# Performance work log

Hardware: AMD Instinct MI355X
Metric: run time of the kernel (lower is better)

Reference implementation:

```python
import jax, jax.numpy as jnp
import numpy as np

MASK_RADIUS = 30.0

def _lowpass_mask(H, W):
    cht, cwt = H // 2, W // 2
    fy = jnp.arange(H, dtype=jnp.float32)[:, None]
    fx = jnp.arange(W, dtype=jnp.float32)[None, :]
    dist = jnp.sqrt((fx - cwt) ** 2 + (fy - cht) ** 2)
    return (dist <= MASK_RADIUS).astype(jnp.float32)

def setup_inputs() -> dict:
    key = jax.random.key(0)
    k1, k2, k3 = jax.random.split(key, 3)
    x = jax.random.normal(k1, (16, 64, 128, 128), dtype=jnp.float32)
    weight = jax.random.normal(k2, (64, 64, 3, 3), dtype=jnp.float32)
    bias = jax.random.normal(k3, (64,), dtype=jnp.float32)
    return {"x": x, "weight": weight, "bias": bias}

def reference(x, weight, bias):
    B, Cin, H, W = x.shape
    # torch.fft.fftshift default shifts ALL dims; jnp default matches.
    fft_x = jnp.fft.fftshift(jnp.fft.fft2(x))                    # [B,Cin,H,W] complex
    kernel_fft = jnp.fft.fftshift(jnp.fft.fft2(weight, s=(H, W)))  # [Cout,Cin,H,W] complex
    # low-pass filter in the shifted frequency domain
    fft_x = fft_x * _lowpass_mask(H, W)
    # channel mixing = batched complex GEMM per frequency (avoids [B,Cout,Cin,H,W] intermediate)
    fft_out = jnp.einsum('bihw,oihw->bohw', fft_x, kernel_fft)
    out = jnp.fft.ifft2(jnp.fft.ifftshift(fft_out, axes=(-2, -1)), axes=(-2, -1)).real
    return out + bias[None, :, None, None]
```

## Files before the change

kernel.cpp:

```cpp
#include <hip/hip_runtime.h>


#define PI2_128 0.04908738521234052f
#define NF 1891

typedef __attribute__((ext_vector_type(8))) short bf16x8;
typedef __attribute__((ext_vector_type(4))) float f32x4;

__device__ const int k_flist[64] = {
    2, 6, 10, 14, 18, 22, 26, 30, 34, 38, 42, 46, 50, 54, 58,
    3, 7, 11, 15, 19, 23, 27, 31, 35, 39, 43, 47, 51, 55, 59,
    0, 4, 8, 12, 16, 20, 24, 28, 32, 36, 40, 44, 48, 52, 56, 60,
    1, 5, 9, 13, 17, 21, 25, 29, 33, 37, 41, 45, 49, 53, 57,
    0, 0, 0};

__device__ inline unsigned bf16_rne(float v) {
  unsigned u = __float_as_uint(v);
  return (u + 0x7FFFu + ((u >> 16) & 1u)) >> 16;
}

__device__ inline bf16x8 mk_bf16x8(unsigned a, unsigned b, unsigned c, unsigned d) {
  union { unsigned u[4]; bf16x8 v; } x;
  x.u[0] = a; x.u[1] = b; x.u[2] = c; x.u[3] = d;
  return x.v;
}

__global__ __launch_bounds__(256) void k0_what(const float* __restrict__ w,
                                               unsigned* __restrict__ Wt) {
  const int tid = threadIdx.x;
  const int fxp = blockIdx.x >> 4;
  const int ig = blockIdx.x & 15;
  const int il = tid & 3;
  const int o = ((tid >> 5) << 3) | ((tid >> 2) & 7);
  const int i = ig * 4 + il;
  const int op = (o + 32) & 63;
  const float* wp = w + (size_t)(op * 64 + i) * 9;
  float w9[9];
#pragma unroll
  for (int k = 0; k < 9; ++k) w9[k] = wp[k];

  const float fx = (float)(fxp - 30);
  float sn, cs;
  __sincosf(fx * PI2_128, &sn, &cs);
  const float e1x = cs, e1y = -sn;
  const float e2x = e1x * e1x - e1y * e1y, e2y = 2.f * e1x * e1y;
  float rxr[3], rxi[3];
#pragma unroll
  for (int ky = 0; ky < 3; ++ky) {
    rxr[ky] = w9[ky * 3] + w9[ky * 3 + 1] * e1x + w9[ky * 3 + 2] * e2x;
    rxi[ky] = w9[ky * 3 + 1] * e1y + w9[ky * 3 + 2] * e2y;
  }
  float pyx = 1.f, pyy = 0.f;
  const float stx = 0.9987954562f, sty = -0.04906767433f;
  unsigned* Wb = Wt + (size_t)(fxp * 31) * 4096 + (o >> 3) * 512 + (i >> 4) * 128 +
                 (((i >> 2) & 3) * 8 + (o & 7)) * 4 + (i & 3);
  for (int fy = 0; fy < 31; ++fy) {
    float p2x = pyx * pyx - pyy * pyy, p2y = 2.f * pyx * pyy;
    float Wre = rxr[0] + (rxr[1] * pyx - rxi[1] * pyy) + (rxr[2] * p2x - rxi[2] * p2y);
    float Wim = rxi[0] + (rxr[1] * pyy + rxi[1] * pyx) + (rxr[2] * p2y + rxi[2] * p2x);
    Wb[(size_t)fy * 4096] = bf16_rne(Wre) | (bf16_rne(Wim) << 16);
    float nx = pyx * stx - pyy * sty;
    pyy = pyx * sty + pyy * stx;
    pyx = nx;
  }
}

__global__ __launch_bounds__(256) void k12_fwd(const float* __restrict__ x,
                                               float* __restrict__ X2) {
  __shared__ __align__(16) float Cls[8968];
  const int bi = blockIdx.x;
  const int tid = threadIdx.x;
  const float* img = x + (size_t)bi * 16384;

  {
    const int tg = tid >> 5;
    const int xg = tid & 31;
    const int t_[4] = {4 * tg, 4 * tg + 2, 2 * tg + 1, 2 * tg + 17};
    const float sgn = (tg & 1) ? 1.f : -1.f;
    float pc[4], ps[4], stc[4], sts[4];
#pragma unroll
    for (int f = 0; f < 4; ++f) {
      __sincosf((float)t_[f] * PI2_128, &sts[f], &stc[f]);
      pc[f] = 1.f;
      ps[f] = 0.f;
    }
    float ar_[4][4] = {{0.f}}, ai_[4][4] = {{0.f}};
    for (int y = 0; y < 32; ++y) {
      float v[4][4];
#pragma unroll
      for (int k = 0; k < 4; ++k)
#pragma unroll
        for (int m = 0; m < 4; ++m) v[k][m] = img[(y + 32 * k) * 128 + xg + 32 * m];
#pragma unroll
      for (int m = 0; m < 4; ++m) {
        float s = v[0][m] + v[2][m], d = v[0][m] - v[2][m];
        float s2 = v[1][m] + v[3][m], d2 = (v[1][m] - v[3][m]) * sgn;
        float a0 = s + s2, a1 = s - s2;
        ar_[0][m] += a0 * pc[0];
        ai_[0][m] -= a0 * ps[0];
        ar_[1][m] += a1 * pc[1];
        ai_[1][m] -= a1 * ps[1];
        ar_[2][m] += d * pc[2] + d2 * ps[2];
        ai_[2][m] += -d * ps[2] + d2 * pc[2];
        ar_[3][m] += d * pc[3] + d2 * ps[3];
        ai_[3][m] += -d * ps[3] + d2 * pc[3];
      }
#pragma unroll
      for (int f = 0; f < 4; ++f) {
        float c = pc[f], s = ps[f];
        pc[f] = c * stc[f] - s * sts[f];
        ps[f] = s * stc[f] + c * sts[f];
      }
    }
#pragma unroll
    for (int f = 0; f < 4; ++f) {
      int t = t_[f];
      float Ar = ar_[f][0] + ar_[f][2], Ai = ai_[f][0] + ai_[f][2];
      float Br = ar_[f][0] - ar_[f][2], Bi = ai_[f][0] - ai_[f][2];
      float Cr = ar_[f][1] + ar_[f][3], Ci = ai_[f][1] + ai_[f][3];
      float Dr = ar_[f][1] - ar_[f][3], Di = ai_[f][1] - ai_[f][3];
      float* base = Cls + xg * 70 + 2 * t;
      *(float2*)(base + 0 * 2244) = make_float2(Ar + Cr, Ai + Ci);
      *(float2*)(base + 1 * 2244) = make_float2(Br + Di, Bi - Dr);
      *(float2*)(base + 2 * 2244) = make_float2(Ar - Cr, Ai - Ci);
      *(float2*)(base + 3 * 2244) = make_float2(Br - Di, Bi + Dr);
    }
  }
  __syncthreads();

  {
    const int tg2 = tid >> 5;
    const int fxg = tid & 31;
    float accr[2][4] = {{0.f}}, acci[2][4] = {{0.f}};
    int fxp_[2], r_[2];
    float pc2[2], ps2[2], stc2[2], sts2[2];
#pragma unroll
    for (int u = 0; u < 2; ++u) {
      fxp_[u] = k_flist[2 * fxg + u];
      r_[u] = (fxp_[u] + 2) & 3;
      float fx = (float)(fxp_[u] - 30);
      __sincosf(fx * PI2_128, &sts2[u], &stc2[u]);
      pc2[u] = 1.f;
      ps2[u] = 0.f;
    }
    for (int xx = 0; xx < 32; ++xx) {
#pragma unroll
      for (int u = 0; u < 2; ++u) {
        const float* bp = Cls + r_[u] * 2244 + xx * 70 + 8 * tg2;
        float2 p0 = *(const float2*)(bp);
        float2 p1 = *(const float2*)(bp + 2);
        float2 p2 = *(const float2*)(bp + 4);
        float2 p3 = *(const float2*)(bp + 6);
        float zr[4] = {p0.x, p1.x, p2.x, p3.x};
        float zi[4] = {p0.y, p1.y, p2.y, p3.y};
        float c = pc2[u], s = ps2[u];
#pragma unroll
        for (int tt = 0; tt < 4; ++tt) {
          accr[u][tt] += zr[tt] * c + zi[tt] * s;
          acci[u][tt] += zi[tt] * c - zr[tt] * s;
        }
        pc2[u] = c * stc2[u] - s * sts2[u];
        ps2[u] = s * stc2[u] + c * sts2[u];
      }
    }
    float2* X2c = (float2*)X2 + (size_t)bi * NF;
#pragma unroll
    for (int u = 0; u < 2; ++u) {
      if (2 * fxg + u >= 61) continue;
      int fxp = fxp_[u], fx = fxp - 30;
#pragma unroll
      for (int tt = 0; tt < 4; ++tt) {
        int t = 4 * tg2 + tt;
        if (t >= 31) continue;
        bool keep = (t * t + fx * fx) <= 900;
        X2c[fxp * 31 + t] =
            keep ? make_float2(accr[u][tt], acci[u][tt]) : make_float2(0.f, 0.f);
      }
    }
  }
}

__global__ __launch_bounds__(256) void ktx(const float2* __restrict__ X2,
                                           float2* __restrict__ X2T) {
  __shared__ __align__(16) float2 Ld[4096];
  const int tid = threadIdx.x;
  const int tf = blockIdx.x % 30;
  const int tc = blockIdx.x / 30;
  const int f2_0 = tf * 64;
  const int lo = tid & 63, hi = tid >> 6;
#pragma unroll
  for (int k = 0; k < 16; ++k) {
    int c = k * 4 + hi;
    int bi = (c & 15) * 64 + tc * 4 + (c >> 4);
    int f2 = f2_0 + lo;
    float2 v = (f2 < NF) ? X2[(size_t)bi * NF + f2] : make_float2(0.f, 0.f);
    Ld[(c << 6) | (lo ^ c)] = v;
  }
  __syncthreads();
#pragma unroll
  for (int k = 0; k < 16; ++k) {
    int fr = k * 4 + hi;
    int f2 = f2_0 + fr;
    if (f2 < NF) X2T[(size_t)f2 * 1024 + tc * 64 + lo] = Ld[(lo << 6) | (fr ^ lo)];
  }
}

__global__ __launch_bounds__(256) void k3_mfma(const float* X2T,
                                               const unsigned* __restrict__ WtB,
                                               float* F) {
  const int nwg = (int)gridDim.x;
  const int orig = (int)blockIdx.x;
  const int xcd = orig & 7;
  const int q = nwg >> 3, r = nwg & 7;
  const int blk = (xcd < r ? xcd * (q + 1) : r * (q + 1) + (xcd - r) * q) + (orig >> 3);

  const int tid = (int)threadIdx.x;
  const int wv = tid >> 6;
  const int g = blk * 4 + wv;
  const int f2v = g >> 1;
  const bool valid = f2v < NF;
  const int f2 = valid ? f2v : NF - 1;
  const int half = g & 1;
  const int lane = tid & 63;
  const int m = lane & 15;
  const int lg = lane >> 4;
  const int bs = (m + 8) & 15;
  const int co = m & 1;

  float2 xv[4][4];
  const float2* Xc = (const float2*)X2T;
#pragma unroll
  for (int ks = 0; ks < 4; ++ks)
#pragma unroll
    for (int t = 0; t < 4; ++t)
      xv[ks][t] = Xc[(size_t)f2 * 1024 + (ks * 16 + lg * 4 + t) * 16 + bs];

  __syncthreads();

  unsigned ahi[4][4], alo[4][4];
#pragma unroll
  for (int ks = 0; ks < 4; ++ks) {
#pragma unroll
    for (int t = 0; t < 4; ++t) {
      float xr = xv[ks][t].x, xi = xv[ks][t].y;
      unsigned hr = bf16_rne(xr), hi2 = bf16_rne(xi);
      float lr = xr - __uint_as_float(hr << 16);
      float li = xi - __uint_as_float(hi2 << 16);
      ahi[ks][t] = hr | (hi2 << 16);
      alo[ks][t] = bf16_rne(lr) | (bf16_rne(li) << 16);
    }
  }

  f32x4 acc[4];
#pragma unroll
  for (int nt = 0; nt < 4; ++nt) acc[nt] = {0.f, 0.f, 0.f, 0.f};

  const unsigned* Wb =
      WtB + (size_t)f2 * 4096 + half * 2048 + (lg * 8 + (m >> 1)) * 4;
#pragma unroll
  for (int ks = 0; ks < 4; ++ks) {
    bf16x8 bfr[4];
#pragma unroll
    for (int nt = 0; nt < 4; ++nt) {
      uint4 wq = *(const uint4*)(Wb + nt * 512 + ks * 128);
      unsigned b0, b1, b2, b3;
      if (co) {
        b0 = (wq.x >> 16) | (wq.x << 16);
        b1 = (wq.y >> 16) | (wq.y << 16);
        b2 = (wq.z >> 16) | (wq.z << 16);
        b3 = (wq.w >> 16) | (wq.w << 16);
      } else {
        b0 = wq.x ^ 0x80000000u;
        b1 = wq.y ^ 0x80000000u;
        b2 = wq.z ^ 0x80000000u;
        b3 = wq.w ^ 0x80000000u;
      }
      bfr[nt] = mk_bf16x8(b0, b1, b2, b3);
    }
    bf16x8 ah = mk_bf16x8(ahi[ks][0], ahi[ks][1], ahi[ks][2], ahi[ks][3]);
    bf16x8 al = mk_bf16x8(alo[ks][0], alo[ks][1], alo[ks][2], alo[ks][3]);
#pragma unroll
    for (int nt = 0; nt < 4; ++nt)
      acc[nt] = __builtin_amdgcn_mfma_f32_16x16x32_bf16(ah, bfr[nt], acc[nt], 0, 0, 0);
#pragma unroll
    for (int nt = 0; nt < 4; ++nt)
      acc[nt] = __builtin_amdgcn_mfma_f32_16x16x32_bf16(al, bfr[nt], acc[nt], 0, 0, 0);
  }

  if (valid) {
    float* Fo = F + (size_t)f2 * 2048 + half * 64 + m;
#pragma unroll
    for (int nt = 0; nt < 4; ++nt)
#pragma unroll
      for (int rr = 0; rr < 4; ++rr)
        Fo[(lg * 4 + rr) * 128 + nt * 16] = acc[nt][rr];
  }
}

__global__ __launch_bounds__(256) void ktf(const float2* __restrict__ F2,
                                           float2* __restrict__ FT) {
  __shared__ __align__(16) float2 Ld[4096];
  const int tid = threadIdx.x;
  const int tf = blockIdx.x % 30;
  const int tc = blockIdx.x / 30;
  const int f2_0 = tf * 64, c0 = tc * 64;
  const int lo = tid & 63, hi = tid >> 6;
#pragma unroll
  for (int k = 0; k < 16; ++k) {
    int fr = k * 4 + hi;
    int f2 = f2_0 + fr;
    float2 v = (f2 < NF) ? F2[(size_t)f2 * 1024 + c0 + lo] : make_float2(0.f, 0.f);
    Ld[(fr << 6) | (lo ^ fr)] = v;
  }
  __syncthreads();
#pragma unroll
  for (int k = 0; k < 16; ++k) {
    int cc = k * 4 + hi;
    int f2 = f2_0 + lo;
    if (f2 < NF) FT[(size_t)(c0 + cc) * NF + f2] = Ld[(lo << 6) | (cc ^ lo)];
  }
}

__global__ __launch_bounds__(256) void k45_out(const float* __restrict__ FT,
                                               const float* __restrict__ bias,
                                               float* __restrict__ out) {
  __shared__ __align__(16) float2 tw[128];
  __shared__ __align__(16) float U[61 * 132];
  __shared__ __align__(16) float TF[3904];
  const int b = blockIdx.x >> 6;
  const int o = blockIdx.x & 63;
  const int tid = threadIdx.x;
  float2* Fl = (float2*)TF;
  const float2* Fc = (const float2*)FT + (size_t)(b * 64 + o) * NF;
  if (tid < 128) {
    float sv, cv;
    __sincosf((float)tid * PI2_128, &sv, &cv);
    tw[tid] = make_float2(cv, sv);
  }
  for (int j = tid; j < NF; j += 256) Fl[j] = Fc[j];
  __syncthreads();

  {
    const int fy = tid & 31;
    const int xg = tid >> 3 >> 2;
    if (fy < 31) {
      float Sr[4][4] = {{0.f}}, Si[4][4] = {{0.f}};
      float pr[4], pi[4], cr[4], ci[4];
#pragma unroll
      for (int j = 0; j < 4; ++j) {
        int xj = 4 * xg + j;
        float2 st = tw[xj];
        cr[j] = st.x;
        ci[j] = st.y;
        float2 p0 = tw[(-30 * xj) & 127];
        pr[j] = p0.x;
        pi[j] = p0.y;
      }
      const float2* Frow = Fl + fy;
      for (int f4 = 0; f4 < 60; f4 += 4) {
#pragma unroll
        for (int ss = 0; ss < 4; ++ss) {
          const int r = (ss + 2) & 3;
          float2 fv = Frow[(f4 + ss) * 31];
#pragma unroll
          for (int j = 0; j < 4; ++j) {
            Sr[r][j] += fv.x * pr[j] - fv.y * pi[j];
            Si[r][j] += fv.x * pi[j] + fv.y * pr[j];
            float np = pr[j] * cr[j] - pi[j] * ci[j];
            pi[j] = pi[j] * cr[j] + pr[j] * ci[j];
            pr[j] = np;
          }
        }
      }
      {
        float2 fv = Frow[60 * 31];
#pragma unroll
        for (int j = 0; j < 4; ++j) {
          Sr[2][j] += fv.x * pr[j] - fv.y * pi[j];
          Si[2][j] += fv.x * pi[j] + fv.y * pr[j];
        }
      }
#pragma unroll
      for (int j = 0; j < 4; ++j) {
        int xj = 4 * xg + j;
        float Er = Sr[0][j] + Sr[2][j], Ei = Si[0][j] + Si[2][j];
        float Fr = Sr[0][j] - Sr[2][j], Fi = Si[0][j] - Si[2][j];
        float Gr = Sr[1][j] + Sr[3][j], Gi = Si[1][j] + Si[3][j];
        float Hr = Sr[1][j] - Sr[3][j], Hi = Si[1][j] - Si[3][j];
        U[fy * 132 + xj] = Er + Gr;
        U[fy * 132 + xj + 32] = Fr - Hi;
        U[fy * 132 + xj + 64] = Er - Gr;
        U[fy * 132 + xj + 96] = Fr + Hi;
        if (fy >= 1) {
          U[(30 + fy) * 132 + xj] = Ei + Gi;
          U[(30 + fy) * 132 + xj + 32] = Fi + Hr;
          U[(30 + fy) * 132 + xj + 64] = Ei - Gi;
          U[(30 + fy) * 132 + xj + 96] = Fi - Hr;
        }
      }
    }
  }
  __syncthreads();
  {
    const float sc1 = 1.f / 16384.f;
    float* T = TF;
    for (int j = tid; j < 61 * 64; j += 256) {
      int c = j >> 6, y = j & 63;
      float val;
      if (c == 0) val = sc1;
      else if (c <= 30) val = 2.f * sc1 * tw[(c * y) & 127].x;
      else val = -2.f * sc1 * tw[((c - 30) * y) & 127].y;
      T[j] = val;
    }
  }
  __syncthreads();
  {
    const float* T = TF;
    const int yg = tid >> 5;
    const int xg = tid & 31;
    const int y0 = yg * 8, x0 = xg * 4;
    float Pa[8][4] = {{0.f}}, Qa[8][4] = {{0.f}};
    for (int c = 0; c < 60; c += 2) {
      float tf0[8], tf1[8], uf0[4], uf1[4];
      *(float4*)&tf0[0] = *(const float4*)(&T[c * 64 + y0]);
      *(float4*)&tf0[4] = *(const float4*)(&T[c * 64 + y0 + 4]);
      *(float4*)&tf1[0] = *(const float4*)(&T[(c + 1) * 64 + y0]);
      *(float4*)&tf1[4] = *(const float4*)(&T[(c + 1) * 64 + y0 + 4]);
      *(float4*)&uf0[0] = *(const float4*)(&U[c * 132 + x0]);
      *(float4*)&uf1[0] = *(const float4*)(&U[(c + 1) * 132 + x0]);
#pragma unroll
      for (int jy = 0; jy < 8; ++jy)
#pragma unroll
        for (int jx = 0; jx < 4; ++jx) {
          Pa[jy][jx] += tf0[jy] * uf0[jx];
          Qa[jy][jx] += tf1[jy] * uf1[jx];
        }
    }
    {
      float tf0[8], uf0[4];
      *(float4*)&tf0[0] = *(const float4*)(&T[60 * 64 + y0]);
      *(float4*)&tf0[4] = *(const float4*)(&T[60 * 64 + y0 + 4]);
      *(float4*)&uf0[0] = *(const float4*)(&U[60 * 132 + x0]);
#pragma unroll
      for (int jy = 0; jy < 8; ++jy)
#pragma unroll
        for (int jx = 0; jx < 4; ++jx) Pa[jy][jx] += tf0[jy] * uf0[jx];
    }
    const float bo_ = bias[o];
    float* op = out + (size_t)(b * 64 + o) * 16384;
#pragma unroll
    for (int jy = 0; jy < 8; ++jy) {
      float4 lo, hi;
      lo.x = Pa[jy][0] + Qa[jy][0] + bo_;
      lo.y = Pa[jy][1] + Qa[jy][1] + bo_;
      lo.z = Pa[jy][2] + Qa[jy][2] + bo_;
      lo.w = Pa[jy][3] + Qa[jy][3] + bo_;
      hi.x = Pa[jy][0] - Qa[jy][0] + bo_;
      hi.y = Pa[jy][1] - Qa[jy][1] + bo_;
      hi.z = Pa[jy][2] - Qa[jy][2] + bo_;
      hi.w = Pa[jy][3] - Qa[jy][3] + bo_;
      *(float4*)(op + (y0 + jy) * 128 + x0) = lo;
      *(float4*)(op + (y0 + jy + 64) * 128 + x0) = hi;
    }
  }
}

extern "C" void kernel_launch(void* const* d_in, const int* in_sizes, int n_in,
                              void* d_out, int out_size, void* d_ws, size_t ws_size,
                              hipStream_t stream) {
  (void)in_sizes; (void)n_in; (void)out_size; (void)ws_size;
  const float* x = (const float*)d_in[0];
  const float* w = (const float*)d_in[1];
  const float* bias = (const float*)d_in[2];
  float* out = (float*)d_out;

  unsigned* Wt = (unsigned*)d_ws;
  float* A = (float*)d_ws + 7745536;
  float* B = (float*)d_ws + 11618304;

  k0_what<<<976, 256, 0, stream>>>(w, Wt);
  k12_fwd<<<1024, 256, 0, stream>>>(x, A);
  ktx<<<480, 256, 0, stream>>>((const float2*)A, (float2*)B);
  k3_mfma<<<946, 256, 0, stream>>>(B, Wt, B);
  ktf<<<480, 256, 0, stream>>>((const float2*)B, (float2*)A);
  k45_out<<<1024, 256, 0, stream>>>(A, bias, out);
}
```

Measured before the change: 226.3 us.

## Stage radix-4 butterfly inputs in LDS with float4 loads in forward FFT

The first stage of the forward column DFT used to have every thread read 16 scalar global values per row and redo the radix-4 butterflies redundantly across the 8 thread groups. Now the image is loaded cooperatively with float4 loads in two halves, butterflied once, and the even and odd partial sums are stored in shared memory. The per-frequency accumulation then reads those from LDS. This cuts redundant global loads and arithmetic, at the cost of extra barriers and LDS traffic, and it reuses the shared buffer before the later stage.

New measurement: 238.2 us. 5.3% more time.

```diff
diff --git a/kernel.cpp b/kernel.cpp
--- a/kernel.cpp
+++ b/kernel.cpp
@@ -67,64 +67,110 @@
 
 __global__ __launch_bounds__(256) void k12_fwd(const float* __restrict__ x,
                                                float* __restrict__ X2) {
-  __shared__ __align__(16) float Cls[8968];
+  __shared__ __align__(16) float SMEM[8968];
   const int bi = blockIdx.x;
   const int tid = threadIdx.x;
   const float* img = x + (size_t)bi * 16384;
 
-  {
-    const int tg = tid >> 5;
-    const int xg = tid & 31;
-    const int t_[4] = {4 * tg, 4 * tg + 2, 2 * tg + 1, 2 * tg + 17};
-    const float sgn = (tg & 1) ? 1.f : -1.f;
-    float pc[4], ps[4], stc[4], sts[4];
-#pragma unroll
-    for (int f = 0; f < 4; ++f) {
-      __sincosf((float)t_[f] * PI2_128, &sts[f], &stc[f]);
-      pc[f] = 1.f;
-      ps[f] = 0.f;
-    }
-    float ar_[4][4] = {{0.f}}, ai_[4][4] = {{0.f}};
-    for (int y = 0; y < 32; ++y) {
-      float v[4][4];
-#pragma unroll
-      for (int k = 0; k < 4; ++k)
-#pragma unroll
-        for (int m = 0; m < 4; ++m) v[k][m] = img[(y + 32 * k) * 128 + xg + 32 * m];
-#pragma unroll
-      for (int m = 0; m < 4; ++m) {
-        float s = v[0][m] + v[2][m], d = v[0][m] - v[2][m];
-        float s2 = v[1][m] + v[3][m], d2 = (v[1][m] - v[3][m]) * sgn;
-        float a0 = s + s2, a1 = s - s2;
-        ar_[0][m] += a0 * pc[0];
-        ai_[0][m] -= a0 * ps[0];
-        ar_[1][m] += a1 * pc[1];
-        ai_[1][m] -= a1 * ps[1];
-        ar_[2][m] += d * pc[2] + d2 * ps[2];
-        ai_[2][m] += -d * ps[2] + d2 * pc[2];
-        ar_[3][m] += d * pc[3] + d2 * ps[3];
-        ai_[3][m] += -d * ps[3] + d2 * pc[3];
-      }
-#pragma unroll
-      for (int f = 0; f < 4; ++f) {
-        float c = pc[f], s = ps[f];
-        pc[f] = c * stc[f] - s * sts[f];
-        ps[f] = s * stc[f] + c * sts[f];
-      }
-    }
-#pragma unroll
-    for (int f = 0; f < 4; ++f) {
-      int t = t_[f];
-      float Ar = ar_[f][0] + ar_[f][2], Ai = ai_[f][0] + ai_[f][2];
-      float Br = ar_[f][0] - ar_[f][2], Bi = ai_[f][0] - ai_[f][2];
-      float Cr = ar_[f][1] + ar_[f][3], Ci = ai_[f][1] + ai_[f][3];
-      float Dr = ar_[f][1] - ar_[f][3], Di = ai_[f][1] - ai_[f][3];
-      float* base = Cls + xg * 70 + 2 * t;
-      *(float2*)(base + 0 * 2244) = make_float2(Ar + Cr, Ai + Ci);
-      *(float2*)(base + 1 * 2244) = make_float2(Br + Di, Bi - Dr);
-      *(float2*)(base + 2 * 2244) = make_float2(Ar - Cr, Ai - Ci);
-      *(float2*)(base + 3 * 2244) = make_float2(Br - Di, Bi + Dr);
-    }
+  float2* Ep = (float2*)SMEM;
+  float2* Op = (float2*)SMEM + 2048;
+
+  const int tg = tid >> 5;
+  const int xg = tid & 31;
+  const int t_[4] = {4 * tg, 4 * tg + 2, 2 * tg + 1, 2 * tg + 17};
+  const float sgn = (tg & 1) ? 1.f : -1.f;
+  float stc[4], sts[4];
+#pragma unroll
+  for (int f = 0; f < 4; ++f) __sincosf((float)t_[f] * PI2_128, &sts[f], &stc[f]);
+
+  float ar_[4][4] = {{0.f}}, ai_[4][4] = {{0.f}};
+
+  const int yq = tid >> 3, xl = tid & 7;
+  for (int h = 0; h < 2; ++h) {
+#pragma unroll
+    for (int c = 0; c < 2; ++c) {
+      const int x0 = h * 64 + xl * 4 + c * 32;
+      const float* p = img + yq * 128 + x0;
+      float4 v0 = *(const float4*)(p);
+      float4 v1 = *(const float4*)(p + 32 * 128);
+      float4 v2 = *(const float4*)(p + 64 * 128);
+      float4 v3 = *(const float4*)(p + 96 * 128);
+      const int xloc = xl * 4 + c * 32;
+      float2* Eb = Ep + yq * 64 + xloc;
+      float2* Ob = Op + yq * 64 + xloc;
+      {
+        float s = v0.x + v2.x, s2 = v1.x + v3.x;
+        Eb[0] = make_float2(s + s2, s - s2);
+        Ob[0] = make_float2(v0.x - v2.x, v1.x - v3.x);
+      }
+      {
+        float s = v0.y + v2.y, s2 = v1.y + v3.y;
+        Eb[1] = make_float2(s + s2, s - s2);
+        Ob[1] = make_float2(v0.y - v2.y, v1.y - v3.y);
+      }
+      {
+        float s = v0.z + v2.z, s2 = v1.z + v3.z;
+        Eb[2] = make_float2(s + s2, s - s2);
+        Ob[2] = make_float2(v0.z - v2.z, v1.z - v3.z);
+      }
+      {
+        float s = v0.w + v2.w, s2 = v1.w + v3.w;
+        Eb[3] = make_float2(s + s2, s - s2);
+        Ob[3] = make_float2(v0.w - v2.w, v1.w - v3.w);
+      }
+    }
+    __syncthreads();
+
+    {
+      float pc[4] = {1.f, 1.f, 1.f, 1.f}, ps[4] = {0.f, 0.f, 0.f, 0.f};
+      const int m0 = 2 * h, m1 = 2 * h + 1;
+      for (int y = 0; y < 32; ++y) {
+        float2 e0 = Ep[y * 64 + xg];
+        float2 e1 = Ep[y * 64 + xg + 32];
+        float2 o0 = Op[y * 64 + xg];
+        float2 o1 = Op[y * 64 + xg + 32];
+        float sps2 = sgn * ps[2], spc2 = sgn * pc[2];
+        float sps3 = sgn * ps[3], spc3 = sgn * pc[3];
+        ar_[0][m0] += e0.x * pc[0];
+        ai_[0][m0] -= e0.x * ps[0];
+        ar_[1][m0] += e0.y * pc[1];
+        ai_[1][m0] -= e0.y * ps[1];
+        ar_[2][m0] += o0.x * pc[2] + o0.y * sps2;
+        ai_[2][m0] += -o0.x * ps[2] + o0.y * spc2;
+        ar_[3][m0] += o0.x * pc[3] + o0.y * sps3;
+        ai_[3][m0] += -o0.x * ps[3] + o0.y * spc3;
+        ar_[0][m1] += e1.x * pc[0];
+        ai_[0][m1] -= e1.x * ps[0];
+        ar_[1][m1] += e1.y * pc[1];
+        ai_[1][m1] -= e1.y * ps[1];
+        ar_[2][m1] += o1.x * pc[2] + o1.y * sps2;
+        ai_[2][m1] += -o1.x * ps[2] + o1.y * spc2;
+        ar_[3][m1] += o1.x * pc[3] + o1.y * sps3;
+        ai_[3][m1] += -o1.x * ps[3] + o1.y * spc3;
+#pragma unroll
+        for (int f = 0; f < 4; ++f) {
+          float c = pc[f], s = ps[f];
+          pc[f] = c * stc[f] - s * sts[f];
+          ps[f] = s * stc[f] + c * sts[f];
+        }
+      }
+    }
+    __syncthreads();
+  }
+
+  float* Cls = SMEM;
+#pragma unroll
+  for (int f = 0; f < 4; ++f) {
+    int t = t_[f];
+    float Ar = ar_[f][0] + ar_[f][2], Ai = ai_[f][0] + ai_[f][2];
+    float Br = ar_[f][0] - ar_[f][2], Bi = ai_[f][0] - ai_[f][2];
+    float Cr = ar_[f][1] + ar_[f][3], Ci = ai_[f][1] + ai_[f][3];
+    float Dr = ar_[f][1] - ar_[f][3], Di = ai_[f][1] - ai_[f][3];
+    float* base = Cls + xg * 70 + 2 * t;
+    *(float2*)(base + 0 * 2244) = make_float2(Ar + Cr, Ai + Ci);
+    *(float2*)(base + 1 * 2244) = make_float2(Br + Di, Bi - Dr);
+    *(float2*)(base + 2 * 2244) = make_float2(Ar - Cr, Ai - Ci);
+    *(float2*)(base + 3 * 2244) = make_float2(Br - Di, Bi + Dr);
   }
   __syncthreads();
 
```

## Split forward DFT over two blocks per image and swizzle shared-memory layout

Applied to the files above, without the earlier changes.

The forward row/column DFT kernel now launches two blocks per image, each computing half of the retained row frequencies (16 of 31). This halves per-thread accumulators and shared memory and doubles the grid to improve occupancy and latency hiding. The shared buffer switches to an XOR-swizzled float2 layout to avoid bank conflicts. The cost is that each image's input is read twice from global memory and the first-stage butterfly work is duplicated.

Measured after the change: 342.8 us. 51.5% more time.

```diff
diff --git a/kernel.cpp b/kernel.cpp
--- a/kernel.cpp
+++ b/kernel.cpp
@@ -67,24 +67,26 @@
 
 __global__ __launch_bounds__(256) void k12_fwd(const float* __restrict__ x,
                                                float* __restrict__ X2) {
-  __shared__ __align__(16) float Cls[8968];
-  const int bi = blockIdx.x;
+  __shared__ __align__(16) float2 Cls[2064];
+  const int bi = blockIdx.x >> 1;
+  const int th = blockIdx.x & 1;
   const int tid = threadIdx.x;
   const float* img = x + (size_t)bi * 16384;
 
+  const int tg = tid >> 5;
+  const int xg = tid & 31;
+
   {
-    const int tg = tid >> 5;
-    const int xg = tid & 31;
-    const int t_[4] = {4 * tg, 4 * tg + 2, 2 * tg + 1, 2 * tg + 17};
+    const int te = 16 * th + 2 * tg;
+    const int to = te + 1;
     const float sgn = (tg & 1) ? 1.f : -1.f;
-    float pc[4], ps[4], stc[4], sts[4];
-#pragma unroll
-    for (int f = 0; f < 4; ++f) {
-      __sincosf((float)t_[f] * PI2_128, &sts[f], &stc[f]);
-      pc[f] = 1.f;
-      ps[f] = 0.f;
-    }
-    float ar_[4][4] = {{0.f}}, ai_[4][4] = {{0.f}};
+    const bool e_hi = (tg & 1) != 0;
+    float stcE, stsE, stcO, stsO;
+    __sincosf((float)te * PI2_128, &stsE, &stcE);
+    __sincosf((float)to * PI2_128, &stsO, &stcO);
+    float pcE = 1.f, psE = 0.f, pcO = 1.f, psO = 0.f;
+    float arE[4] = {0.f, 0.f, 0.f, 0.f}, aiE[4] = {0.f, 0.f, 0.f, 0.f};
+    float arO[4] = {0.f, 0.f, 0.f, 0.f}, aiO[4] = {0.f, 0.f, 0.f, 0.f};
     for (int y = 0; y < 32; ++y) {
       float v[4][4];
 #pragma unroll
@@ -96,85 +98,81 @@
         float s = v[0][m] + v[2][m], d = v[0][m] - v[2][m];
         float s2 = v[1][m] + v[3][m], d2 = (v[1][m] - v[3][m]) * sgn;
         float a0 = s + s2, a1 = s - s2;
-        ar_[0][m] += a0 * pc[0];
-        ai_[0][m] -= a0 * ps[0];
-        ar_[1][m] += a1 * pc[1];
-        ai_[1][m] -= a1 * ps[1];
-        ar_[2][m] += d * pc[2] + d2 * ps[2];
-        ai_[2][m] += -d * ps[2] + d2 * pc[2];
-        ar_[3][m] += d * pc[3] + d2 * ps[3];
-        ai_[3][m] += -d * ps[3] + d2 * pc[3];
-      }
-#pragma unroll
-      for (int f = 0; f < 4; ++f) {
-        float c = pc[f], s = ps[f];
-        pc[f] = c * stc[f] - s * sts[f];
-        ps[f] = s * stc[f] + c * sts[f];
-      }
-    }
-#pragma unroll
-    for (int f = 0; f < 4; ++f) {
-      int t = t_[f];
-      float Ar = ar_[f][0] + ar_[f][2], Ai = ai_[f][0] + ai_[f][2];
-      float Br = ar_[f][0] - ar_[f][2], Bi = ai_[f][0] - ai_[f][2];
-      float Cr = ar_[f][1] + ar_[f][3], Ci = ai_[f][1] + ai_[f][3];
-      float Dr = ar_[f][1] - ar_[f][3], Di = ai_[f][1] - ai_[f][3];
-      float* base = Cls + xg * 70 + 2 * t;
-      *(float2*)(base + 0 * 2244) = make_float2(Ar + Cr, Ai + Ci);
-      *(float2*)(base + 1 * 2244) = make_float2(Br + Di, Bi - Dr);
-      *(float2*)(base + 2 * 2244) = make_float2(Ar - Cr, Ai - Ci);
-      *(float2*)(base + 3 * 2244) = make_float2(Br - Di, Bi + Dr);
+        float ae = e_hi ? a1 : a0;
+        arE[m] += ae * pcE;
+        aiE[m] -= ae * psE;
+        arO[m] += d * pcO + d2 * psO;
+        aiO[m] += -d * psO + d2 * pcO;
+      }
+      {
+        float c = pcE, s = psE;
+        pcE = c * stcE - s * stsE;
+        psE = s * stcE + c * stsE;
+      }
+      {
+        float c = pcO, s = psO;
+        pcO = c * stcO - s * stsO;
+        psO = s * stcO + c * stsO;
+      }
+    }
+#pragma unroll
+    for (int f = 0; f < 2; ++f) {
+      const float* ar_ = f ? arO : arE;
+      const float* ai_ = f ? aiO : aiE;
+      const int tloc = 2 * tg + f;
+      float Ar = ar_[0] + ar_[2], Ai = ai_[0] + ai_[2];
+      float Br = ar_[0] - ar_[2], Bi = ai_[0] - ai_[2];
+      float Cr = ar_[1] + ar_[3], Ci = ai_[1] + ai_[3];
+      float Dr = ar_[1] - ar_[3], Di = ai_[1] - ai_[3];
+      const int s = tloc ^ (xg & 15);
+      const int rowb = xg * 16 + s;
+      Cls[0 * 516 + rowb] = make_float2(Ar + Cr, Ai + Ci);
+      Cls[1 * 516 + rowb] = make_float2(Br + Di, Bi - Dr);
+      Cls[2 * 516 + rowb] = make_float2(Ar - Cr, Ai - Ci);
+      Cls[3 * 516 + rowb] = make_float2(Br - Di, Bi + Dr);
     }
   }
   __syncthreads();
 
   {
-    const int tg2 = tid >> 5;
+    const int tq = (tid >> 5) & 3;
+    const int ub = tid >> 7;
     const int fxg = tid & 31;
-    float accr[2][4] = {{0.f}}, acci[2][4] = {{0.f}};
-    int fxp_[2], r_[2];
-    float pc2[2], ps2[2], stc2[2], sts2[2];
-#pragma unroll
-    for (int u = 0; u < 2; ++u) {
-      fxp_[u] = k_flist[2 * fxg + u];
-      r_[u] = (fxp_[u] + 2) & 3;
-      float fx = (float)(fxp_[u] - 30);
-      __sincosf(fx * PI2_128, &sts2[u], &stc2[u]);
-      pc2[u] = 1.f;
-      ps2[u] = 0.f;
-    }
+    const int li = 2 * fxg + ub;
+    const int fxp = k_flist[li];
+    const int r = (fxp + 2) & 3;
+    float stc2, sts2;
+    __sincosf((float)(fxp - 30) * PI2_128, &sts2, &stc2);
+    float pc2 = 1.f, ps2 = 0.f;
+    float accr[4] = {0.f, 0.f, 0.f, 0.f}, acci[4] = {0.f, 0.f, 0.f, 0.f};
+    const int ts4 = 4 * tq;
     for (int xx = 0; xx < 32; ++xx) {
-#pragma unroll
-      for (int u = 0; u < 2; ++u) {
-        const float* bp = Cls + r_[u] * 2244 + xx * 70 + 8 * tg2;
-        float2 p0 = *(const float2*)(bp);
-        float2 p1 = *(const float2*)(bp + 2);
-        float2 p2 = *(const float2*)(bp + 4);
-        float2 p3 = *(const float2*)(bp + 6);
-        float zr[4] = {p0.x, p1.x, p2.x, p3.x};
-        float zi[4] = {p0.y, p1.y, p2.y, p3.y};
-        float c = pc2[u], s = ps2[u];
-#pragma unroll
-        for (int tt = 0; tt < 4; ++tt) {
-          accr[u][tt] += zr[tt] * c + zi[tt] * s;
-          acci[u][tt] += zi[tt] * c - zr[tt] * s;
-        }
-        pc2[u] = c * stc2[u] - s * sts2[u];
-        ps2[u] = s * stc2[u] + c * sts2[u];
-      }
-    }
-    float2* X2c = (float2*)X2 + (size_t)bi * NF;
-#pragma unroll
-    for (int u = 0; u < 2; ++u) {
-      if (2 * fxg + u >= 61) continue;
-      int fxp = fxp_[u], fx = fxp - 30;
+      const float2* bp = Cls + r * 516 + xx * 16;
+      const int s0 = ts4 ^ (xx & 15);
+      float2 p0 = bp[s0];
+      float2 p1 = bp[s0 ^ 1];
+      float2 p2 = bp[s0 ^ 2];
+      float2 p3 = bp[s0 ^ 3];
+      float zr[4] = {p0.x, p1.x, p2.x, p3.x};
+      float zi[4] = {p0.y, p1.y, p2.y, p3.y};
+      float c = pc2, s = ps2;
 #pragma unroll
       for (int tt = 0; tt < 4; ++tt) {
-        int t = 4 * tg2 + tt;
-        if (t >= 31) continue;
+        accr[tt] += zr[tt] * c + zi[tt] * s;
+        acci[tt] += zi[tt] * c - zr[tt] * s;
+      }
+      pc2 = c * stc2 - s * sts2;
+      ps2 = s * stc2 + c * sts2;
+    }
+    if (li < 61) {
+      float2* X2c = (float2*)X2 + (size_t)bi * NF;
+      const int fx = fxp - 30;
+#pragma unroll
+      for (int tt = 0; tt < 4; ++tt) {
+        int t = 16 * th + ts4 + tt;
+        if (t > 30) continue;
         bool keep = (t * t + fx * fx) <= 900;
-        X2c[fxp * 31 + t] =
-            keep ? make_float2(accr[u][tt], acci[u][tt]) : make_float2(0.f, 0.f);
+        X2c[fxp * 31 + t] = keep ? make_float2(accr[tt], acci[tt]) : make_float2(0.f, 0.f);
       }
     }
   }
@@ -479,7 +477,7 @@
   float* B = (float*)d_ws + 11618304;
 
   k0_what<<<976, 256, 0, stream>>>(w, Wt);
-  k12_fwd<<<1024, 256, 0, stream>>>(x, A);
+  k12_fwd<<<2048, 256, 0, stream>>>(x, A);
   ktx<<<480, 256, 0, stream>>>((const float2*)A, (float2*)B);
   k3_mfma<<<946, 256, 0, stream>>>(B, Wt, B);
   ktf<<<480, 256, 0, stream>>>((const float2*)B, (float2*)A);
```
